# Performance work log

Hardware: AMD Instinct MI355X
Metric: run time of the kernel (lower is better)

Reference implementation:

```python
import jax, jax.numpy as jnp
import numpy as np

TOP_K = 2  # num_active_experts


def setup_inputs() -> dict:
    key = jax.random.key(0)
    k1, k2, k3 = jax.random.split(key, 3)
    N, D, E = 16384, 1024, 8
    x = jax.random.normal(k1, (N, D), dtype=jnp.float32)
    router_w = jax.random.normal(k2, (E, D), dtype=jnp.float32) * (1.0 / np.sqrt(D))
    router_b = jnp.zeros((E,), dtype=jnp.float32)
    expert_w = jax.random.normal(k3, (E, D, D), dtype=jnp.float32) * (1.0 / np.sqrt(D))
    expert_b = jnp.zeros((E, D), dtype=jnp.float32)
    return {"x": x, "router_w": router_w, "router_b": router_b,
            "expert_w": expert_w, "expert_b": expert_b}


def reference(x, router_w, router_b, expert_w, expert_b):
    E = router_w.shape[0]
    # Router: softmax over experts, pick top-k, renormalize
    logits = x @ router_w.T + router_b                      # [N, E]
    probs = jax.nn.softmax(logits, axis=-1)                 # [N, E]
    top_p, top_i = jax.lax.top_k(probs, TOP_K)              # [N, K]
    top_p = top_p / jnp.sum(top_p, axis=-1, keepdims=True)  # renormalized gates
    # Dense combine weights: [N, E], zero for non-selected experts
    combine = jnp.sum(jax.nn.one_hot(top_i, E, dtype=x.dtype) * top_p[..., None], axis=1)
    # All-expert outputs, then weighted combine (vectorized dispatch/combine)
    y = jnp.einsum('nd,eod->neo', x, expert_w) + expert_b   # [N, E, O]
    out = jnp.einsum('neo,ne->no', y, combine)              # [N, O]
    return out
```

## Files before the change

kernel.cpp:

```cpp
#include <hip/hip_runtime.h>
#include <hip/hip_bf16.h>


constexpr int DIMS = 1024;
constexpr int NE   = 8;

typedef __attribute__((ext_vector_type(8))) short short8;
typedef __attribute__((ext_vector_type(4))) float f32x4;

typedef const __attribute__((address_space(1))) void* gp_t;
typedef __attribute__((address_space(3))) void* sp_t;

__device__ __forceinline__ float b2f(unsigned short u) {
  union { unsigned int i; float f; } x; x.i = ((unsigned)u) << 16; return x.f;
}

__global__ __launch_bounds__(256) void wconv_kernel(const float* __restrict__ w,
                                                    __hip_bfloat16* __restrict__ wb) {
  size_t i = (size_t)blockIdx.x * 256 + threadIdx.x;
  const float4* w4 = (const float4*)w;
  float4 a = w4[i * 2], b = w4[i * 2 + 1];
  union { __hip_bfloat16 h[8]; float4 f; } u;
  u.h[0] = __float2bfloat16(a.x); u.h[1] = __float2bfloat16(a.y);
  u.h[2] = __float2bfloat16(a.z); u.h[3] = __float2bfloat16(a.w);
  u.h[4] = __float2bfloat16(b.x); u.h[5] = __float2bfloat16(b.y);
  u.h[6] = __float2bfloat16(b.z); u.h[7] = __float2bfloat16(b.w);
  ((float4*)wb)[i] = u.f;
}

__global__ __launch_bounds__(256) void router_kernel(
    const float* __restrict__ x, const float* __restrict__ rw,
    const float* __restrict__ rb, __hip_bfloat16* __restrict__ xb,
    int* __restrict__ counts, int* __restrict__ entries,
    float* __restrict__ gates, int n_tok) {
  __shared__ float s_rw[NE * DIMS];
  __shared__ int s_cnt[NE], s_base[NE];
  __shared__ int s_e[32];
  __shared__ float s_g[32];
  __shared__ int s_pos[32];
  const int tid = threadIdx.x;

  const float4* rw4 = (const float4*)rw;
  float4* s4 = (float4*)s_rw;
  for (int i = tid; i < NE * DIMS / 4; i += 256) s4[i] = rw4[i];
  if (tid < NE) s_cnt[tid] = 0;
  __syncthreads();

  const int wave = tid >> 6, lane = tid & 63;
  for (int i = 0; i < 4; ++i) {
    int t = blockIdx.x * 16 + wave * 4 + i;
    float a[NE];
#pragma unroll
    for (int e = 0; e < NE; ++e) a[e] = 0.f;
#pragma unroll
    for (int j = 0; j < DIMS / 64; ++j) {
      int d = lane + j * 64;
      float v = x[(size_t)t * DIMS + d];
      xb[(size_t)t * DIMS + d] = __float2bfloat16(v);
#pragma unroll
      for (int e = 0; e < NE; ++e) a[e] = fmaf(v, s_rw[e * DIMS + d], a[e]);
    }
    double da[NE];
#pragma unroll
    for (int e = 0; e < NE; ++e) da[e] = (double)a[e];
#pragma unroll
    for (int off = 32; off > 0; off >>= 1) {
#pragma unroll
      for (int e = 0; e < NE; ++e) da[e] += __shfl_xor(da[e], off, 64);
    }
    if (lane == 0) {
      float l[NE];
#pragma unroll
      for (int e = 0; e < NE; ++e) l[e] = (float)da[e] + rb[e];
      int e0 = 0;
#pragma unroll
      for (int e = 1; e < NE; ++e) if (l[e] > l[e0]) e0 = e;
      int e1 = (e0 == 0) ? 1 : 0;
#pragma unroll
      for (int e = 0; e < NE; ++e) if (e != e0 && l[e] > l[e1]) e1 = e;
      float r = expf(l[e1] - l[e0]);
      float g0 = 1.f / (1.f + r);
      float g1 = 1.f - g0;
      int ai = (wave * 4 + i) * 2;
      int p0 = atomicAdd(&s_cnt[e0], 1);
      int p1 = atomicAdd(&s_cnt[e1], 1);
      s_e[ai] = e0; s_g[ai] = g0; s_pos[ai] = p0;
      s_e[ai + 1] = e1; s_g[ai + 1] = g1; s_pos[ai + 1] = p1;
    }
  }
  __syncthreads();
  if (tid < NE) s_base[tid] = atomicAdd(&counts[tid], s_cnt[tid]);
  __syncthreads();
  if (tid < 32) {
    int e = s_e[tid];
    int p = s_base[e] + s_pos[tid];
    int tok = blockIdx.x * 16 + (tid >> 1);
    entries[e * n_tok + p] = (tok << 1) | (tid & 1);
    gates[e * n_tok + p] = s_g[tid];
  }
}

__global__ __launch_bounds__(256) void moe_gemm(
    const __hip_bfloat16* __restrict__ xb, const __hip_bfloat16* __restrict__ wb,
    const float* __restrict__ eb, const int* __restrict__ counts,
    const int* __restrict__ entries, const float* __restrict__ gates,
    __hip_bfloat16* __restrict__ y, int n_tok) {
  int e = -1, rt = 0, cnt = 0, acc_t = 0;
#pragma unroll
  for (int i = 0; i < NE; ++i) {
    int c = counts[i];
    int t = (c + 127) >> 7;
    if (e < 0 && (int)blockIdx.y < acc_t + t) { e = i; rt = (int)blockIdx.y - acc_t; cnt = c; }
    acc_t += t;
  }
  if (e < 0) return;

  __shared__ __hip_bfloat16 As[128 * 32];
  __shared__ __hip_bfloat16 Bs[128 * 32];

  const int tid = threadIdx.x;
  const int lane = tid & 63, wave = tid >> 6;
  const int row0 = rt * 128;
  const int n0 = blockIdx.x * 128;

  const int rA0 = tid >> 2, rA1 = rA0 + 64;
  const int kcol = (tid & 3) * 8;
  int gr0 = row0 + rA0, gr1 = row0 + rA1;
  int ent0 = (gr0 < cnt) ? entries[e * n_tok + gr0] : 0;
  int ent1 = (gr1 < cnt) ? entries[e * n_tok + gr1] : 0;
  const __hip_bfloat16* ap0 = xb + (size_t)(ent0 >> 1) * DIMS + kcol;
  const __hip_bfloat16* ap1 = xb + (size_t)(ent1 >> 1) * DIMS + kcol;
  const __hip_bfloat16* wbase = wb + (size_t)e * DIMS * DIMS;
  const __hip_bfloat16* bp0 = wbase + (size_t)(n0 + rA0) * DIMS + kcol;
  const __hip_bfloat16* bp1 = wbase + (size_t)(n0 + rA1) * DIMS + kcol;
  __hip_bfloat16* sA0 = As + tid * 8;
  __hip_bfloat16* sA1 = As + (tid + 256) * 8;
  __hip_bfloat16* sB0 = Bs + tid * 8;
  __hip_bfloat16* sB1 = Bs + (tid + 256) * 8;

  f32x4 acc[4][4] = {};

  const int wm = (wave & 1) * 64, wn = (wave >> 1) * 64;
  const int fr = lane & 15, fko = (lane >> 4) * 8;

  for (int k0 = 0; k0 < DIMS; k0 += 32) {
    __builtin_amdgcn_global_load_lds((gp_t)(ap0 + k0), (sp_t)sA0, 16, 0, 0);
    __builtin_amdgcn_global_load_lds((gp_t)(ap1 + k0), (sp_t)sA1, 16, 0, 0);
    __builtin_amdgcn_global_load_lds((gp_t)(bp0 + k0), (sp_t)sB0, 16, 0, 0);
    __builtin_amdgcn_global_load_lds((gp_t)(bp1 + k0), (sp_t)sB1, 16, 0, 0);
    __syncthreads();
    short8 af[4], bf[4];
#pragma unroll
    for (int mt = 0; mt < 4; ++mt)
      af[mt] = *(const short8*)&As[(wm + mt * 16 + fr) * 32 + fko];
#pragma unroll
    for (int nt = 0; nt < 4; ++nt)
      bf[nt] = *(const short8*)&Bs[(wn + nt * 16 + fr) * 32 + fko];
#pragma unroll
    for (int mt = 0; mt < 4; ++mt)
#pragma unroll
      for (int nt = 0; nt < 4; ++nt)
        acc[mt][nt] = __builtin_amdgcn_mfma_f32_16x16x32_bf16(af[mt], bf[nt], acc[mt][nt], 0, 0, 0);
    __syncthreads();
  }

  const int quad = lane >> 4;
  float bias[4];
#pragma unroll
  for (int nt = 0; nt < 4; ++nt) bias[nt] = eb[e * DIMS + n0 + wn + nt * 16 + fr];
#pragma unroll
  for (int mt = 0; mt < 4; ++mt) {
#pragma unroll
    for (int r = 0; r < 4; ++r) {
      int m = wm + mt * 16 + quad * 4 + r;
      int gr = row0 + m;
      if (gr < cnt) {
        int ent = entries[e * n_tok + gr];
        float g = gates[e * n_tok + gr];
        __hip_bfloat16* yp = y + (size_t)ent * DIMS + n0 + wn + fr;
#pragma unroll
        for (int nt = 0; nt < 4; ++nt)
          yp[nt * 16] = __float2bfloat16(g * (acc[mt][nt][r] + bias[nt]));
      }
    }
  }
}

__global__ __launch_bounds__(256) void combine_kernel(const __hip_bfloat16* __restrict__ y,
                                                      float* __restrict__ out) {
  size_t idx = (size_t)blockIdx.x * 256 + threadIdx.x;
  size_t n = idx >> 7;
  int c = (int)(idx & 127) << 3;
  short8 v0 = *(const short8*)(y + (n * 2) * DIMS + c);
  short8 v1 = *(const short8*)(y + (n * 2 + 1) * DIMS + c);
  float4 o0, o1;
  o0.x = b2f((unsigned short)v0[0]) + b2f((unsigned short)v1[0]);
  o0.y = b2f((unsigned short)v0[1]) + b2f((unsigned short)v1[1]);
  o0.z = b2f((unsigned short)v0[2]) + b2f((unsigned short)v1[2]);
  o0.w = b2f((unsigned short)v0[3]) + b2f((unsigned short)v1[3]);
  o1.x = b2f((unsigned short)v0[4]) + b2f((unsigned short)v1[4]);
  o1.y = b2f((unsigned short)v0[5]) + b2f((unsigned short)v1[5]);
  o1.z = b2f((unsigned short)v0[6]) + b2f((unsigned short)v1[6]);
  o1.w = b2f((unsigned short)v0[7]) + b2f((unsigned short)v1[7]);
  float* op = out + n * DIMS + c;
  ((float4*)op)[0] = o0;
  ((float4*)op)[1] = o1;
}

extern "C" void kernel_launch(void* const* d_in, const int* in_sizes, int n_in,
                              void* d_out, int out_size, void* d_ws, size_t ws_size,
                              hipStream_t stream) {
  const float* x  = (const float*)d_in[0];
  const float* rw = (const float*)d_in[1];
  const float* rb = (const float*)d_in[2];
  const float* ew = (const float*)d_in[3];
  const float* eb = (const float*)d_in[4];
  float* out = (float*)d_out;
  const int n_tok = in_sizes[0] / DIMS;

  char* ws = (char*)d_ws;
  size_t off = 0;
  int* counts = (int*)ws;                      off += 256;
  __hip_bfloat16* xb = (__hip_bfloat16*)(ws + off); off += (size_t)n_tok * DIMS * 2;
  __hip_bfloat16* wb = (__hip_bfloat16*)(ws + off); off += (size_t)NE * DIMS * DIMS * 2;
  int*   entries = (int*)(ws + off);           off += (size_t)NE * n_tok * 4;
  float* gates   = (float*)(ws + off);         off += (size_t)NE * n_tok * 4;
  __hip_bfloat16* y = (__hip_bfloat16*)(ws + off); off += (size_t)n_tok * 2 * DIMS * 2;
  if (ws_size < off) return;

  hipMemsetAsync(counts, 0, 256, stream);
  wconv_kernel<<<NE * DIMS * DIMS / (8 * 256), 256, 0, stream>>>(ew, wb);
  router_kernel<<<n_tok / 16, 256, 0, stream>>>(x, rw, rb, xb, counts, entries, gates, n_tok);
  dim3 g(DIMS / 128, 2 * n_tok / 128 + NE);
  moe_gemm<<<g, 256, 0, stream>>>(xb, wb, eb, counts, entries, gates, y, n_tok);
  combine_kernel<<<(unsigned)((size_t)n_tok * DIMS / 8 / 256), 256, 0, stream>>>(y, out);
}
```

Before: 292.1 us.

## Merge weight conversion into router kernel and load two K-slices per barrier

```diff
diff --git a/kernel.cpp b/kernel.cpp
--- a/kernel.cpp
+++ b/kernel.cpp
@@ -4,6 +4,8 @@
 
 constexpr int DIMS = 1024;
 constexpr int NE   = 8;
+constexpr int ROUTER_BLOCKS = 1024;
+constexpr int WCONV_BLOCKS  = NE * DIMS * DIMS / (8 * 256);
 
 typedef __attribute__((ext_vector_type(8))) short short8;
 typedef __attribute__((ext_vector_type(4))) float f32x4;
@@ -15,30 +17,32 @@
   union { unsigned int i; float f; } x; x.i = ((unsigned)u) << 16; return x.f;
 }
 
-__global__ __launch_bounds__(256) void wconv_kernel(const float* __restrict__ w,
-                                                    __hip_bfloat16* __restrict__ wb) {
-  size_t i = (size_t)blockIdx.x * 256 + threadIdx.x;
-  const float4* w4 = (const float4*)w;
-  float4 a = w4[i * 2], b = w4[i * 2 + 1];
-  union { __hip_bfloat16 h[8]; float4 f; } u;
-  u.h[0] = __float2bfloat16(a.x); u.h[1] = __float2bfloat16(a.y);
-  u.h[2] = __float2bfloat16(a.z); u.h[3] = __float2bfloat16(a.w);
-  u.h[4] = __float2bfloat16(b.x); u.h[5] = __float2bfloat16(b.y);
-  u.h[6] = __float2bfloat16(b.z); u.h[7] = __float2bfloat16(b.w);
-  ((float4*)wb)[i] = u.f;
-}
-
-__global__ __launch_bounds__(256) void router_kernel(
+__global__ __launch_bounds__(256) void prep_kernel(
     const float* __restrict__ x, const float* __restrict__ rw,
-    const float* __restrict__ rb, __hip_bfloat16* __restrict__ xb,
+    const float* __restrict__ rb, const float* __restrict__ ew,
+    __hip_bfloat16* __restrict__ xb, __hip_bfloat16* __restrict__ wb,
     int* __restrict__ counts, int* __restrict__ entries,
     float* __restrict__ gates, int n_tok) {
+  const int tid = threadIdx.x;
+
+  if ((int)blockIdx.x >= ROUTER_BLOCKS) {
+    size_t i = (size_t)(blockIdx.x - ROUTER_BLOCKS) * 256 + tid;
+    const float4* w4 = (const float4*)ew;
+    float4 a = w4[i * 2], b = w4[i * 2 + 1];
+    union { __hip_bfloat16 h[8]; float4 f; } u;
+    u.h[0] = __float2bfloat16(a.x); u.h[1] = __float2bfloat16(a.y);
+    u.h[2] = __float2bfloat16(a.z); u.h[3] = __float2bfloat16(a.w);
+    u.h[4] = __float2bfloat16(b.x); u.h[5] = __float2bfloat16(b.y);
+    u.h[6] = __float2bfloat16(b.z); u.h[7] = __float2bfloat16(b.w);
+    ((float4*)wb)[i] = u.f;
+    return;
+  }
+
   __shared__ float s_rw[NE * DIMS];
   __shared__ int s_cnt[NE], s_base[NE];
   __shared__ int s_e[32];
   __shared__ float s_g[32];
   __shared__ int s_pos[32];
-  const int tid = threadIdx.x;
 
   const float4* rw4 = (const float4*)rw;
   float4* s4 = (float4*)s_rw;
@@ -115,8 +119,8 @@
   }
   if (e < 0) return;
 
-  __shared__ __hip_bfloat16 As[128 * 32];
-  __shared__ __hip_bfloat16 Bs[128 * 32];
+  __shared__ __hip_bfloat16 As[2][128 * 32];
+  __shared__ __hip_bfloat16 Bs[2][128 * 32];
 
   const int tid = threadIdx.x;
   const int lane = tid & 63, wave = tid >> 6;
@@ -133,34 +137,36 @@
   const __hip_bfloat16* wbase = wb + (size_t)e * DIMS * DIMS;
   const __hip_bfloat16* bp0 = wbase + (size_t)(n0 + rA0) * DIMS + kcol;
   const __hip_bfloat16* bp1 = wbase + (size_t)(n0 + rA1) * DIMS + kcol;
-  __hip_bfloat16* sA0 = As + tid * 8;
-  __hip_bfloat16* sA1 = As + (tid + 256) * 8;
-  __hip_bfloat16* sB0 = Bs + tid * 8;
-  __hip_bfloat16* sB1 = Bs + (tid + 256) * 8;
 
   f32x4 acc[4][4] = {};
 
   const int wm = (wave & 1) * 64, wn = (wave >> 1) * 64;
   const int fr = lane & 15, fko = (lane >> 4) * 8;
 
-  for (int k0 = 0; k0 < DIMS; k0 += 32) {
-    __builtin_amdgcn_global_load_lds((gp_t)(ap0 + k0), (sp_t)sA0, 16, 0, 0);
-    __builtin_amdgcn_global_load_lds((gp_t)(ap1 + k0), (sp_t)sA1, 16, 0, 0);
-    __builtin_amdgcn_global_load_lds((gp_t)(bp0 + k0), (sp_t)sB0, 16, 0, 0);
-    __builtin_amdgcn_global_load_lds((gp_t)(bp1 + k0), (sp_t)sB1, 16, 0, 0);
+  for (int k0 = 0; k0 < DIMS; k0 += 64) {
+#pragma unroll
+    for (int s = 0; s < 2; ++s) {
+      __builtin_amdgcn_global_load_lds((gp_t)(ap0 + k0 + s * 32), (sp_t)(As[s] + tid * 8), 16, 0, 0);
+      __builtin_amdgcn_global_load_lds((gp_t)(ap1 + k0 + s * 32), (sp_t)(As[s] + (tid + 256) * 8), 16, 0, 0);
+      __builtin_amdgcn_global_load_lds((gp_t)(bp0 + k0 + s * 32), (sp_t)(Bs[s] + tid * 8), 16, 0, 0);
+      __builtin_amdgcn_global_load_lds((gp_t)(bp1 + k0 + s * 32), (sp_t)(Bs[s] + (tid + 256) * 8), 16, 0, 0);
+    }
     __syncthreads();
-    short8 af[4], bf[4];
-#pragma unroll
-    for (int mt = 0; mt < 4; ++mt)
-      af[mt] = *(const short8*)&As[(wm + mt * 16 + fr) * 32 + fko];
-#pragma unroll
-    for (int nt = 0; nt < 4; ++nt)
-      bf[nt] = *(const short8*)&Bs[(wn + nt * 16 + fr) * 32 + fko];
-#pragma unroll
-    for (int mt = 0; mt < 4; ++mt)
+#pragma unroll
+    for (int s = 0; s < 2; ++s) {
+      short8 af[4], bf[4];
+#pragma unroll
+      for (int mt = 0; mt < 4; ++mt)
+        af[mt] = *(const short8*)&As[s][(wm + mt * 16 + fr) * 32 + fko];
 #pragma unroll
       for (int nt = 0; nt < 4; ++nt)
-        acc[mt][nt] = __builtin_amdgcn_mfma_f32_16x16x32_bf16(af[mt], bf[nt], acc[mt][nt], 0, 0, 0);
+        bf[nt] = *(const short8*)&Bs[s][(wn + nt * 16 + fr) * 32 + fko];
+#pragma unroll
+      for (int mt = 0; mt < 4; ++mt)
+#pragma unroll
+        for (int nt = 0; nt < 4; ++nt)
+          acc[mt][nt] = __builtin_amdgcn_mfma_f32_16x16x32_bf16(af[mt], bf[nt], acc[mt][nt], 0, 0, 0);
+    }
     __syncthreads();
   }
 
@@ -229,8 +235,8 @@
   if (ws_size < off) return;
 
   hipMemsetAsync(counts, 0, 256, stream);
-  wconv_kernel<<<NE * DIMS * DIMS / (8 * 256), 256, 0, stream>>>(ew, wb);
-  router_kernel<<<n_tok / 16, 256, 0, stream>>>(x, rw, rb, xb, counts, entries, gates, n_tok);
+  prep_kernel<<<ROUTER_BLOCKS + WCONV_BLOCKS, 256, 0, stream>>>(
+      x, rw, rb, ew, xb, wb, counts, entries, gates, n_tok);
   dim3 g(DIMS / 128, 2 * n_tok / 128 + NE);
   moe_gemm<<<g, 256, 0, stream>>>(xb, wb, eb, counts, entries, gates, y, n_tok);
   combine_kernel<<<(unsigned)((size_t)n_tok * DIMS / 8 / 256), 256, 0, stream>>>(y, out);
```

After: 301.0 us. 1.03x slower.
